# Kernel tuning notes

Hardware: AMD Instinct MI355X
Metric: run time of the kernel (lower is better)

## Reference

```python
import jax, jax.numpy as jnp
import numpy as np

EMBED_LEN = 512
NUM_FEA = 8   # M
NUM_CLS = 14  # C
BETA = 0.3
BATCH = 8192


def setup_inputs() -> dict:
    key = jax.random.key(0)
    k1, k2, k3 = jax.random.split(key, 3)
    x = jax.random.normal(k1, (BATCH, EMBED_LEN * NUM_FEA), dtype=jnp.float32)
    wordvec_array = jax.random.normal(k2, (1, EMBED_LEN, NUM_CLS), dtype=jnp.float32)
    y = jax.random.randint(k3, (BATCH, NUM_CLS), 0, 2, dtype=jnp.int32)
    # guarantee at least one positive and one negative label per sample
    y = y.at[:, 0].set(1).at[:, -1].set(0)
    return {"x": x, "y": y, "wordvec_array": wordvec_array}


def reference(x, y, wordvec_array):
    B = x.shape[0]
    un = x.reshape(B, EMBED_LEN, -1)            # [B, E, M]
    w = wordvec_array[0]                         # [E, C]
    # dot_prod_all[b, c] = max_m <un[b,:,m], w[:,c]>
    dot = jnp.einsum('bem,ec->bmc', un, w).max(axis=1)   # [B, C]

    P = (y == 1).astype(x.dtype)                 # positive mask [B, C]
    N = 1.0 - P                                  # negative mask [B, C]
    npos = P.sum(axis=-1)                        # [B]
    nneg = N.sum(axis=-1)                        # [B]

    # pairwise v[b,p,n] = dot_neg - dot_pos; sum softplus over masked pairs
    V = dot[:, None, :] - dot[:, :, None]        # [B, C(pos), C(neg)]
    pair_sum = jnp.einsum('bp,bn,bpn->b', P, N, jax.nn.softplus(V))
    # edge case: no negatives -> v = -dot_pos
    noneg_sum = jnp.sum(P * jax.nn.softplus(-dot), axis=-1)
    S = jnp.where(nneg > 0, pair_sum, noneg_sum)
    base = S / npos                              # [B]

    # diversity: unbiased variance of positive-class word vectors over class dim
    mean_w = jnp.einsum('bc,ec->be', P, w) / npos[:, None]          # [B, E]
    ss = jnp.einsum('bc,bec->be', P, (w[None] - mean_w[:, :, None]) ** 2)
    var_w = ss / jnp.maximum(npos - 1.0, 1.0)[:, None]
    var_w = jnp.where((npos == 1.0)[:, None], 0.0, var_w)           # sig = 0 if single positive
    total_var = var_w.sum(axis=-1)               # [B]

    # var_regularization: unbiased var over M, L1 over embed dim
    sig2 = jnp.var(un, axis=2, ddof=1)           # [B, E]
    l1_err = jnp.abs(sig2).sum(axis=-1)          # [B]

    # num_fea > 1 branch
    loss = 2.0 * ((1.0 - BETA) * (1.0 + total_var) * base + BETA * l1_err)
    return loss.mean()
```

## Files before the change

### kernel.cpp

```cpp
#include <hip/hip_runtime.h>
#include <math.h>

#define E_LEN 512
#define C_CLS 14
#define BATCH 8192
#define NSLOTS 256
#define WS_G 256
#define WS_WB 464
#define WB_ROW 260
#define NCH 16
#define XKG 72
#define XSLOT 288
#define XBUF 576
#define XW 1152

typedef float v4f __attribute__((ext_vector_type(4)));
typedef short s8v __attribute__((ext_vector_type(8)));
union APk { int i[4]; s8v s; };

#define CVT_PK_BF16(d, a, b) \
  asm("v_cvt_pk_bf16_f32 %0, %1, %2" : "=v"(d) : "v"(a), "v"(b))

__device__ __forceinline__ void dma4(const float* gp, float* lp) {
  __builtin_amdgcn_global_load_lds(
      (const __attribute__((address_space(1))) void*)gp,
      (__attribute__((address_space(3))) void*)lp, 4, 0, 0);
}

template<int CTRL>
__device__ __forceinline__ float dpp_mov_f(float v) {
  return __int_as_float(__builtin_amdgcn_update_dpp(
      0, __float_as_int(v), CTRL, 0xF, 0xF, false));
}
__device__ __forceinline__ float sum16(float v) {
  v += dpp_mov_f<0x128>(v);
  v += dpp_mov_f<0x124>(v);
  v += dpp_mov_f<0x122>(v);
  v += dpp_mov_f<0x121>(v);
  return v;
}
__device__ __forceinline__ float hsum32(float v) {
  v = sum16(v);
  v += dpp_mov_f<0x142>(v);
  return v;
}
__device__ __forceinline__ float wsum64(float v) {
  v = sum16(v);
  v += dpp_mov_f<0x142>(v);
  v += dpp_mov_f<0x143>(v);
  return v;
}
template<int PAT>
__device__ __forceinline__ float swz_f(float v) {
  return __int_as_float(__builtin_amdgcn_ds_swizzle(__float_as_int(v), PAT));
}
__device__ __forceinline__ float shfl_x32(float v) {
  return __shfl_xor(v, 32, 64);
}
__device__ __forceinline__ float softplus_f(float v) {
  return fmaxf(v, 0.f) + __logf(1.f + __expf(-fabsf(v)));
}

__global__ void MID_LOSS_prep(const float* __restrict__ w,
                              float* __restrict__ wsf) {
  __shared__ float wl[E_LEN * C_CLS];
  const int tid = threadIdx.x;
#pragma unroll
  for (int i = 0; i < 7; ++i)
    ((float4*)wl)[tid + i * 256] = ((const float4*)w)[tid + i * 256];
  wsf[tid] = 0.f;
  __syncthreads();
  if (tid < 196) {
    const int p = tid / 14, n = tid - p * 14;
    float g = 0.f;
    for (int e = 0; e < E_LEN; ++e)
      g = fmaf(wl[e * 14 + p], wl[e * 14 + n], g);
    wsf[WS_G + tid] = g;
  }
  unsigned int* wsu = (unsigned int*)wsf;
  for (int i = tid; i < 4096; i += 256) {
    const int c = i >> 8;
    const int ep = i & 255;
    const int e = ep * 2;
    const float v0 = (c < 14) ? wl[e * 14 + c] : 0.f;
    const float v1 = (c < 14) ? wl[(e + 1) * 14 + c] : 0.f;
    int d;
    CVT_PK_BF16(d, v0, v1);
    wsu[WS_WB + c * WB_ROW + ep] = (unsigned int)d;
  }
}

__global__ __launch_bounds__(256, 4)
void MID_LOSS_main(const float* __restrict__ x, const int* __restrict__ y,
                   const float* __restrict__ wsf, float* __restrict__ slots) {
  __shared__ unsigned int wB_l[16 * WB_ROW];
  __shared__ float G_l[196];
  __shared__ alignas(16) float xs[4 * XW];
  __shared__ float dots_l[4][2][16];
  __shared__ float P_l[4][2][16];

  const int tid = threadIdx.x;
  const int lane = tid & 63;
  const int wid = tid >> 6;
  const unsigned int* wsu = (const unsigned int*)wsf;

  for (int i = tid; i < 16 * WB_ROW; i += 256) wB_l[i] = wsu[WS_WB + i];
  if (tid < 196) G_l[tid] = wsf[WS_G + tid];
  __syncthreads();

  const int row = lane & 15;
  const int kg = lane >> 4;
  const int m = row & 7;
  const int b0 = blockIdx.x * 8 + wid * 2;
  const float* xg = x + (size_t)b0 * 4096;
  float* xw = xs + wid * XW;
  const float* xr = xw + (row >> 3) * XSLOT + kg * XKG + m;
  const unsigned int* wrow = wB_l + row * WB_ROW;

#pragma unroll
  for (int c = 0; c < 2; ++c)
#pragma unroll
    for (int sl = 0; sl < 2; ++sl)
#pragma unroll
      for (int kk = 0; kk < 4; ++kk)
        dma4(xg + sl * 4096 + c * 256 + kk * 64 + lane,
             xw + c * XBUF + sl * XSLOT + kk * XKG);

  v4f acc = {0.f, 0.f, 0.f, 0.f};
  v4f acc2 = {0.f, 0.f, 0.f, 0.f};
  float q = 0.f;

#pragma unroll
  for (int ch = 0; ch < NCH; ++ch) {
    const int buf = ch & 1;
    if (ch == NCH - 1)
      asm volatile("s_waitcnt vmcnt(0)" ::: "memory");
    else
      asm volatile("s_waitcnt vmcnt(8)" ::: "memory");

    float u[8];
    const float* xb = xr + buf * XBUF;
#pragma unroll
    for (int j = 0; j < 8; ++j) u[j] = xb[j * 8];
    const s8v bfrag = *(const s8v*)(wrow + ch * 16 + kg * 4);
#pragma unroll
    for (int j = 0; j < 8; ++j) q = fmaf(u[j], u[j], q);
    APk a;
#pragma unroll
    for (int jj = 0; jj < 4; ++jj)
      CVT_PK_BF16(a.i[jj], u[2 * jj], u[2 * jj + 1]);

    if (ch < NCH - 2) {
      asm volatile("s_waitcnt lgkmcnt(0)" ::: "memory");
#pragma unroll
      for (int sl = 0; sl < 2; ++sl)
#pragma unroll
        for (int kk = 0; kk < 4; ++kk)
          dma4(xg + sl * 4096 + (ch + 2) * 256 + kk * 64 + lane,
               xw + buf * XBUF + sl * XSLOT + kk * XKG);
    }

    acc = __builtin_amdgcn_mfma_f32_16x16x32_bf16(a.s, bfrag, acc, 0, 0, 0);
    acc2 = __builtin_amdgcn_mfma_f32_16x16x32_bf16(a.s, a.s, acc2, 0, 0, 0);
  }

  if (lane < 28) {
    const int s = (lane >= 14) ? 1 : 0;
    P_l[wid][s][lane - s * 14] = (y[b0 * 14 + lane] == 1) ? 1.f : 0.f;
  }

  float dmax = fmaxf(fmaxf(acc[0], acc[1]), fmaxf(acc[2], acc[3]));
  dmax = fmaxf(dmax, swz_f<0x401F>(dmax));
  if ((lane & 16) == 0 && (lane & 15) < 14)
    dots_l[wid][lane >> 5][lane & 15] = dmax;

  const float loc2 = acc2[0] + acc2[1] + acc2[2] + acc2[3];
  const bool validb = (((lane & 15) < 8) == (lane < 32));
  float s2v = validb ? loc2 : 0.f;
  float q2 = q + shfl_x32(q);
  float qv = validb ? q2 : 0.f;

  asm volatile("s_waitcnt lgkmcnt(0)" ::: "memory");

  const int half = lane >> 5;
  const int hl = lane & 31;
  const float* dp = dots_l[wid][half];
  const float* Pp = P_l[wid][half];
  float S = 0.f, Gc = 0.f;
#pragma unroll
  for (int r = 0; r < 7; ++r) {
    const int tt = r * 28 + hl;
    if (hl < 28) {
      const int p = (tt * 2341) >> 15;
      const int n = tt - p * 14;
      const float Ppv = Pp[p], Pnv = Pp[n];
      S += Ppv * (1.f - Pnv) * softplus_f(dp[n] - dp[p]);
      Gc = fmaf(Ppv * Pnv, G_l[tt], Gc);
    }
  }
  float npv = (hl < 14) ? Pp[hl] : 0.f;
  float w2v = (hl < 14) ? Pp[hl] * G_l[hl * 15] : 0.f;

  S = hsum32(S);
  Gc = hsum32(Gc);
  s2v = hsum32(s2v);
  qv = hsum32(qv);
  npv = hsum32(npv);
  w2v = hsum32(w2v);

  float loss = 0.f;
  if ((lane & 31) == 31) {
    const float npos = npv;
    const float base = S / npos;
    const float tv =
        (npos > 1.5f) ? (w2v - Gc / npos) / (npos - 1.f) : 0.f;
    const float l1 = (qv - s2v * 0.125f) * (1.f / 7.f);
    loss = 1.4f * (1.f + tv) * base + 0.6f * l1;
  }
  loss += shfl_x32(loss);
  if (lane == 31) atomicAdd(&slots[blockIdx.x & (NSLOTS - 1)], loss);
}

__global__ void MID_LOSS_fin(const float* __restrict__ wsf,
                             float* __restrict__ out) {
  const int tid = threadIdx.x;
  float s = wsf[tid] + wsf[tid + 64] + wsf[tid + 128] + wsf[tid + 192];
  s = wsum64(s);
  if (tid == 63) out[0] = s * (1.f / (float)BATCH);
}

extern "C" void kernel_launch(void* const* d_in, const int* in_sizes, int n_in,
                              void* d_out, int out_size, void* d_ws, size_t ws_size,
                              hipStream_t stream) {
  const float* x = (const float*)d_in[0];
  const int* y = (const int*)d_in[1];
  const float* w = (const float*)d_in[2];
  float* out = (float*)d_out;
  float* wsf = (float*)d_ws;

  MID_LOSS_prep<<<1, 256, 0, stream>>>(w, wsf);
  MID_LOSS_main<<<BATCH / 8, 256, 0, stream>>>(x, y, wsf, wsf);
  MID_LOSS_fin<<<1, 64, 0, stream>>>(wsf, out);
}
```

Measured before the change: 212.6 us.

## Use 16-byte LDS DMA with XOR swizzle and fold final reduction into main kernel

Replaces the per-dword global_load_lds transfers with 16-byte transfers, which cuts the DMA instruction count by four per chunk. An XOR-swizzled source address and read offsets take the place of the padded LDS layout as the way to avoid bank conflicts. The separate finalize kernel is removed: the last block, found through an atomic counter, sums the slots and writes the output, saving one launch. The risks are that the swizzle must exactly match the read pattern, and that the counter-based last-block detection adds fences and atomics to every block.

Result: slower. 239.2 us (+12.5%).

```diff
diff --git a/kernel.cpp b/kernel.cpp
--- a/kernel.cpp
+++ b/kernel.cpp
@@ -5,14 +5,14 @@
 #define C_CLS 14
 #define BATCH 8192
 #define NSLOTS 256
+#define NBLK (BATCH / 8)
 #define WS_G 256
+#define WS_CNT 460
 #define WS_WB 464
 #define WB_ROW 260
 #define NCH 16
-#define XKG 72
-#define XSLOT 288
-#define XBUF 576
-#define XW 1152
+#define XBUF 512
+#define XW 1024
 
 typedef float v4f __attribute__((ext_vector_type(4)));
 typedef short s8v __attribute__((ext_vector_type(8)));
@@ -21,10 +21,10 @@
 #define CVT_PK_BF16(d, a, b) \
   asm("v_cvt_pk_bf16_f32 %0, %1, %2" : "=v"(d) : "v"(a), "v"(b))
 
-__device__ __forceinline__ void dma4(const float* gp, float* lp) {
+__device__ __forceinline__ void dma16(const float* gp, float* lp) {
   __builtin_amdgcn_global_load_lds(
       (const __attribute__((address_space(1))) void*)gp,
-      (__attribute__((address_space(3))) void*)lp, 4, 0, 0);
+      (__attribute__((address_space(3))) void*)lp, 16, 0, 0);
 }
 
 template<int CTRL>
@@ -69,6 +69,7 @@
   for (int i = 0; i < 7; ++i)
     ((float4*)wl)[tid + i * 256] = ((const float4*)w)[tid + i * 256];
   wsf[tid] = 0.f;
+  if (tid == 0) ((unsigned int*)wsf)[WS_CNT] = 0u;
   __syncthreads();
   if (tid < 196) {
     const int p = tid / 14, n = tid - p * 14;
@@ -92,12 +93,14 @@
 
 __global__ __launch_bounds__(256, 4)
 void MID_LOSS_main(const float* __restrict__ x, const int* __restrict__ y,
-                   const float* __restrict__ wsf, float* __restrict__ slots) {
+                   const float* __restrict__ wsf, float* __restrict__ slots,
+                   float* __restrict__ out) {
   __shared__ unsigned int wB_l[16 * WB_ROW];
   __shared__ float G_l[196];
   __shared__ alignas(16) float xs[4 * XW];
   __shared__ float dots_l[4][2][16];
   __shared__ float P_l[4][2][16];
+  __shared__ int lastblk;
 
   const int tid = threadIdx.x;
   const int lane = tid & 63;
@@ -114,17 +117,19 @@
   const int b0 = blockIdx.x * 8 + wid * 2;
   const float* xg = x + (size_t)b0 * 4096;
   float* xw = xs + wid * XW;
-  const float* xr = xw + (row >> 3) * XSLOT + kg * XKG + m;
+
+  const int gsrc = (lane ^ (((lane >> 4) & 3) << 1)) * 4;
+  const float* xr2 = xw + (row >> 3) * 256 + kg * 64 + m;
   const unsigned int* wrow = wB_l + row * WB_ROW;
+  int jo[8];
+#pragma unroll
+  for (int j = 0; j < 8; ++j) jo[j] = 8 * (j ^ kg);
 
 #pragma unroll
   for (int c = 0; c < 2; ++c)
 #pragma unroll
     for (int sl = 0; sl < 2; ++sl)
-#pragma unroll
-      for (int kk = 0; kk < 4; ++kk)
-        dma4(xg + sl * 4096 + c * 256 + kk * 64 + lane,
-             xw + c * XBUF + sl * XSLOT + kk * XKG);
+      dma16(xg + sl * 4096 + c * 256 + gsrc, xw + c * XBUF + sl * 256);
 
   v4f acc = {0.f, 0.f, 0.f, 0.f};
   v4f acc2 = {0.f, 0.f, 0.f, 0.f};
@@ -136,12 +141,12 @@
     if (ch == NCH - 1)
       asm volatile("s_waitcnt vmcnt(0)" ::: "memory");
     else
-      asm volatile("s_waitcnt vmcnt(8)" ::: "memory");
+      asm volatile("s_waitcnt vmcnt(2)" ::: "memory");
 
     float u[8];
-    const float* xb = xr + buf * XBUF;
-#pragma unroll
-    for (int j = 0; j < 8; ++j) u[j] = xb[j * 8];
+    const float* xb = xr2 + buf * XBUF;
+#pragma unroll
+    for (int j = 0; j < 8; ++j) u[j] = xb[jo[j]];
     const s8v bfrag = *(const s8v*)(wrow + ch * 16 + kg * 4);
 #pragma unroll
     for (int j = 0; j < 8; ++j) q = fmaf(u[j], u[j], q);
@@ -154,10 +159,8 @@
       asm volatile("s_waitcnt lgkmcnt(0)" ::: "memory");
 #pragma unroll
       for (int sl = 0; sl < 2; ++sl)
-#pragma unroll
-        for (int kk = 0; kk < 4; ++kk)
-          dma4(xg + sl * 4096 + (ch + 2) * 256 + kk * 64 + lane,
-               xw + buf * XBUF + sl * XSLOT + kk * XKG);
+        dma16(xg + sl * 4096 + (ch + 2) * 256 + gsrc,
+              xw + buf * XBUF + sl * 256);
     }
 
     acc = __builtin_amdgcn_mfma_f32_16x16x32_bf16(a.s, bfrag, acc, 0, 0, 0);
@@ -219,14 +222,22 @@
   }
   loss += shfl_x32(loss);
   if (lane == 31) atomicAdd(&slots[blockIdx.x & (NSLOTS - 1)], loss);
-}
-
-__global__ void MID_LOSS_fin(const float* __restrict__ wsf,
-                             float* __restrict__ out) {
-  const int tid = threadIdx.x;
-  float s = wsf[tid] + wsf[tid + 64] + wsf[tid + 128] + wsf[tid + 192];
-  s = wsum64(s);
-  if (tid == 63) out[0] = s * (1.f / (float)BATCH);
+
+  __syncthreads();
+  if (tid == 0) {
+    __threadfence();
+    const unsigned int old =
+        atomicAdd((unsigned int*)(slots + WS_CNT), 1u);
+    lastblk = (old == (unsigned int)(NBLK - 1)) ? 1 : 0;
+  }
+  __syncthreads();
+  if (lastblk && tid < 64) {
+    float s = atomicAdd(&slots[tid], 0.f) + atomicAdd(&slots[tid + 64], 0.f) +
+              atomicAdd(&slots[tid + 128], 0.f) +
+              atomicAdd(&slots[tid + 192], 0.f);
+    s = wsum64(s);
+    if (tid == 63) out[0] = s * (1.f / (float)BATCH);
+  }
 }
 
 extern "C" void kernel_launch(void* const* d_in, const int* in_sizes, int n_in,
@@ -239,6 +250,5 @@
   float* wsf = (float*)d_ws;
 
   MID_LOSS_prep<<<1, 256, 0, stream>>>(w, wsf);
-  MID_LOSS_main<<<BATCH / 8, 256, 0, stream>>>(x, y, wsf, wsf);
-  MID_LOSS_fin<<<1, 64, 0, stream>>>(wsf, out);
-}
+  MID_LOSS_main<<<NBLK, 256, 0, stream>>>(x, y, wsf, wsf, out);
+}
```

## Replace LDS DMA staging with direct register prefetch of x

Applied to the files above, without the earlier changes.

Removes the global_load_lds double-buffered staging of x through shared memory. Each lane now loads its strided x elements straight into registers, one chunk ahead in a two-deep register buffer. The y load is hoisted ahead of the main loop, and launch bounds are raised to 8 blocks per CU because the kernel needs much less LDS. The direct loads are strided (8 floats apart per lane), so coalescing may be worse than the DMA path, and they depend on the cache to supply the data efficiently.

Measured after the change: 251.7 us. 18.4% more time.

```diff
diff --git a/kernel.cpp b/kernel.cpp
--- a/kernel.cpp
+++ b/kernel.cpp
@@ -5,14 +5,11 @@
 #define C_CLS 14
 #define BATCH 8192
 #define NSLOTS 256
+#define NBLK (BATCH / 8)
 #define WS_G 256
 #define WS_WB 464
 #define WB_ROW 260
 #define NCH 16
-#define XKG 72
-#define XSLOT 288
-#define XBUF 576
-#define XW 1152
 
 typedef float v4f __attribute__((ext_vector_type(4)));
 typedef short s8v __attribute__((ext_vector_type(8)));
@@ -20,12 +17,6 @@
 
 #define CVT_PK_BF16(d, a, b) \
   asm("v_cvt_pk_bf16_f32 %0, %1, %2" : "=v"(d) : "v"(a), "v"(b))
-
-__device__ __forceinline__ void dma4(const float* gp, float* lp) {
-  __builtin_amdgcn_global_load_lds(
-      (const __attribute__((address_space(1))) void*)gp,
-      (__attribute__((address_space(3))) void*)lp, 4, 0, 0);
-}
 
 template<int CTRL>
 __device__ __forceinline__ float dpp_mov_f(float v) {
@@ -90,12 +81,11 @@
   }
 }
 
-__global__ __launch_bounds__(256, 4)
+__global__ __launch_bounds__(256, 8)
 void MID_LOSS_main(const float* __restrict__ x, const int* __restrict__ y,
                    const float* __restrict__ wsf, float* __restrict__ slots) {
   __shared__ unsigned int wB_l[16 * WB_ROW];
   __shared__ float G_l[196];
-  __shared__ alignas(16) float xs[4 * XW];
   __shared__ float dots_l[4][2][16];
   __shared__ float P_l[4][2][16];
 
@@ -112,53 +102,33 @@
   const int kg = lane >> 4;
   const int m = row & 7;
   const int b0 = blockIdx.x * 8 + wid * 2;
-  const float* xg = x + (size_t)b0 * 4096;
-  float* xw = xs + wid * XW;
-  const float* xr = xw + (row >> 3) * XSLOT + kg * XKG + m;
+  const float* xl = x + (size_t)b0 * 4096 + (row >> 3) * 4096 + kg * 64 + m;
   const unsigned int* wrow = wB_l + row * WB_ROW;
 
-#pragma unroll
-  for (int c = 0; c < 2; ++c)
-#pragma unroll
-    for (int sl = 0; sl < 2; ++sl)
-#pragma unroll
-      for (int kk = 0; kk < 4; ++kk)
-        dma4(xg + sl * 4096 + c * 256 + kk * 64 + lane,
-             xw + c * XBUF + sl * XSLOT + kk * XKG);
+  const int yv = (lane < 28) ? y[b0 * 14 + lane] : 0;
 
   v4f acc = {0.f, 0.f, 0.f, 0.f};
   v4f acc2 = {0.f, 0.f, 0.f, 0.f};
   float q = 0.f;
 
+  float u[2][8];
+#pragma unroll
+  for (int j = 0; j < 8; ++j) u[0][j] = xl[j * 8];
+
 #pragma unroll
   for (int ch = 0; ch < NCH; ++ch) {
-    const int buf = ch & 1;
-    if (ch == NCH - 1)
-      asm volatile("s_waitcnt vmcnt(0)" ::: "memory");
-    else
-      asm volatile("s_waitcnt vmcnt(8)" ::: "memory");
-
-    float u[8];
-    const float* xb = xr + buf * XBUF;
-#pragma unroll
-    for (int j = 0; j < 8; ++j) u[j] = xb[j * 8];
+    const int cur = ch & 1;
+    if (ch < NCH - 1) {
+#pragma unroll
+      for (int j = 0; j < 8; ++j) u[cur ^ 1][j] = xl[(ch + 1) * 256 + j * 8];
+    }
     const s8v bfrag = *(const s8v*)(wrow + ch * 16 + kg * 4);
 #pragma unroll
-    for (int j = 0; j < 8; ++j) q = fmaf(u[j], u[j], q);
+    for (int j = 0; j < 8; ++j) q = fmaf(u[cur][j], u[cur][j], q);
     APk a;
 #pragma unroll
     for (int jj = 0; jj < 4; ++jj)
-      CVT_PK_BF16(a.i[jj], u[2 * jj], u[2 * jj + 1]);
-
-    if (ch < NCH - 2) {
-      asm volatile("s_waitcnt lgkmcnt(0)" ::: "memory");
-#pragma unroll
-      for (int sl = 0; sl < 2; ++sl)
-#pragma unroll
-        for (int kk = 0; kk < 4; ++kk)
-          dma4(xg + sl * 4096 + (ch + 2) * 256 + kk * 64 + lane,
-               xw + buf * XBUF + sl * XSLOT + kk * XKG);
-    }
+      CVT_PK_BF16(a.i[jj], u[cur][2 * jj], u[cur][2 * jj + 1]);
 
     acc = __builtin_amdgcn_mfma_f32_16x16x32_bf16(a.s, bfrag, acc, 0, 0, 0);
     acc2 = __builtin_amdgcn_mfma_f32_16x16x32_bf16(a.s, a.s, acc2, 0, 0, 0);
@@ -166,7 +136,7 @@
 
   if (lane < 28) {
     const int s = (lane >= 14) ? 1 : 0;
-    P_l[wid][s][lane - s * 14] = (y[b0 * 14 + lane] == 1) ? 1.f : 0.f;
+    P_l[wid][s][lane - s * 14] = (yv == 1) ? 1.f : 0.f;
   }
 
   float dmax = fmaxf(fmaxf(acc[0], acc[1]), fmaxf(acc[2], acc[3]));
@@ -239,6 +209,6 @@
   float* wsf = (float*)d_ws;
 
   MID_LOSS_prep<<<1, 256, 0, stream>>>(w, wsf);
-  MID_LOSS_main<<<BATCH / 8, 256, 0, stream>>>(x, y, wsf, wsf);
+  MID_LOSS_main<<<NBLK, 256, 0, stream>>>(x, y, wsf, wsf);
   MID_LOSS_fin<<<1, 64, 0, stream>>>(wsf, out);
 }
```
